# Kernel tuning notes

Measured on AMD Instinct MI355X. Metric: run time of the kernel, lower is better.

Reference implementation:

```python
import jax, jax.numpy as jnp
import numpy as np

D_MODEL, D_K, D_V, H = 1024, 64, 64, 16
B, NQ, NK = 4, 2048, 2048


def setup_inputs() -> dict:
    key = jax.random.key(0)
    ks = jax.random.split(key, 14)
    def xavier(k, fan_in, fan_out):
        lim = np.sqrt(6.0 / (fan_in + fan_out))
        return jax.random.uniform(k, (fan_in, fan_out), jnp.float32, -lim, lim)
    return {
        "queries": jax.random.normal(ks[0], (B, NQ, D_MODEL), jnp.float32),
        "keys": jax.random.normal(ks[1], (B, NK, D_MODEL), jnp.float32),
        "values": jax.random.normal(ks[2], (B, NK, D_MODEL), jnp.float32),
        "language_feature": jax.random.normal(ks[3], (B, NQ, D_MODEL), jnp.float32),
        "Wq": xavier(ks[4], D_MODEL, H * D_K), "bq": jnp.zeros((H * D_K,), jnp.float32),
        "Wk": xavier(ks[5], D_MODEL, H * D_K), "bk": jnp.zeros((H * D_K,), jnp.float32),
        "Wv": xavier(ks[6], D_MODEL, H * D_V), "bv": jnp.zeros((H * D_V,), jnp.float32),
        "Ws": xavier(ks[7], D_MODEL, H * D_K), "bs": jnp.zeros((H * D_K,), jnp.float32),
        "Wo": xavier(ks[8], H * D_V, D_MODEL), "bo": jnp.zeros((D_MODEL,), jnp.float32),
    }


def reference(queries, keys, values, language_feature, Wq, bq, Wk, bk, Wv, bv, Ws, bs, Wo, bo):
    b, nq = queries.shape[:2]
    nk = keys.shape[1]
    scale = 1.0 / np.sqrt(D_K)
    # projections -> [b, h, n, d]
    q = (queries @ Wq + bq).reshape(b, nq, H, D_K).transpose(0, 2, 1, 3)
    s = (language_feature @ Ws + bs).reshape(b, nq, H, D_K).transpose(0, 2, 1, 3)
    k = (keys @ Wk + bk).reshape(b, nk, H, D_K).transpose(0, 2, 1, 3)
    v = (values @ Wv + bv).reshape(b, nk, H, D_V).transpose(0, 2, 1, 3)
    # raw scaled scores [b, h, nq, nk]
    att = jnp.einsum("bhqd,bhkd->bhqk", q, k) * scale
    # language branch: per-query dot(q_i, s_i) -> [b, h, nq]
    lang = jnp.einsum("bhqd,bhqd->bhq", q, s) * scale
    # concatenated softmax over [nk + 1]; only last column (beta) is used
    combined = jax.nn.softmax(jnp.concatenate([att, lang[..., None]], axis=-1), axis=-1)
    beta = combined[..., -1:]  # [b, h, nq, 1]
    # NOTE: original uses RAW (non-softmaxed) att for the value aggregation
    att_v = jnp.einsum("bhqk,bhkd->bhqd", att, v)
    out = beta * s + (1.0 - beta) * att_v  # [b, h, nq, d]
    out = out.transpose(0, 2, 1, 3).reshape(b, nq, H * D_V)
    return out @ Wo + bo
```

## Files before the change

kernel.cpp:

```cpp
#include <hip/hip_runtime.h>


#define SCALE 0.125f
#define LOG2E 1.44269504088896f
#define SCLOG 0.18033688011112042f

typedef __attribute__((ext_vector_type(8))) short bf16x8;
typedef __attribute__((ext_vector_type(4))) short s16x4;
typedef __attribute__((ext_vector_type(4))) float f32x4;

__device__ __forceinline__ float b2f(short x) {
  return __uint_as_float(((unsigned)(unsigned short)x) << 16);
}
__device__ __forceinline__ short f2b(float x) {
  unsigned u = __float_as_uint(x);
  unsigned r = (u + 0x7fffu + ((u >> 16) & 1u)) >> 16;
  return (short)r;
}
__device__ __forceinline__ float fexp2(float x) {
  float r;
  asm("v_exp_f32 %0, %1" : "=v"(r) : "v"(x));
  return r;
}
__device__ __forceinline__ bf16x8 cvt8(f32x4 lo, f32x4 hi) {
  unsigned u0, u1, u2, u3;
  asm("v_cvt_pk_bf16_f32 %0, %1, %2" : "=v"(u0) : "v"(lo[0]), "v"(lo[1]));
  asm("v_cvt_pk_bf16_f32 %0, %1, %2" : "=v"(u1) : "v"(lo[2]), "v"(lo[3]));
  asm("v_cvt_pk_bf16_f32 %0, %1, %2" : "=v"(u2) : "v"(hi[0]), "v"(hi[1]));
  asm("v_cvt_pk_bf16_f32 %0, %1, %2" : "=v"(u3) : "v"(hi[2]), "v"(hi[3]));
  union { unsigned u[4]; bf16x8 v; } r;
  r.u[0] = u0; r.u[1] = u1; r.u[2] = u2; r.u[3] = u3;
  return r.v;
}

__device__ __forceinline__ void gl2lds16(const short* g, short* l) {
  __builtin_amdgcn_global_load_lds(
      (const __attribute__((address_space(1))) unsigned int*)g,
      (__attribute__((address_space(3))) unsigned int*)l, 16, 0, 0);
}

__global__ __launch_bounds__(256) void wtrans_kernel(
    const float* W0, const float* W1, const float* W2, const float* W3, const float* W4,
    short* O0, short* O1, short* O2, short* O3, short* O4) {
  const float* Wp[5] = {W0, W1, W2, W3, W4};
  short* Op[5] = {O0, O1, O2, O3, O4};
  const float* W = Wp[blockIdx.z];
  short* O = Op[blockIdx.z];
  int n0 = blockIdx.x * 64, k0 = blockIdx.y * 64;
  __shared__ float ts[64 * 68];
  int tid = threadIdx.x;
  int r = tid >> 4, c = (tid & 15) * 4;
  for (int ir = 0; ir < 4; ++ir) {
    f32x4 v = *reinterpret_cast<const f32x4*>(&W[(size_t)(k0 + r + ir * 16) * 1024 + n0 + c]);
    *reinterpret_cast<f32x4*>(&ts[(r + ir * 16) * 68 + c]) = v;
  }
  __syncthreads();
  for (int ir = 0; ir < 4; ++ir) {
    int n = r + ir * 16;
    s16x4 o;
    for (int j = 0; j < 4; ++j) o[j] = f2b(ts[(c + j) * 68 + n]);
    *reinterpret_cast<s16x4*>(&O[(size_t)(n0 + n) * 1024 + k0 + c]) = o;
  }
}


#define A_LOAD(T, R0, R1, R2, R3)                                           \
  {                                                                         \
    int kst = (T) * 32;                                                     \
    int row0 = tid >> 2, cc0 = tid & 3;                                     \
    int gc0 = (cc0 ^ ((row0 >> 1) & 3)) * 8;                                \
    const float* ap0 = &Ag[(size_t)(m0 + row0) * 1024 + kst + gc0];         \
    R0 = *reinterpret_cast<const f32x4*>(ap0);                              \
    R1 = *reinterpret_cast<const f32x4*>(ap0 + 4);                          \
    int row1 = row0 + 128;                                                  \
    int gc1 = (cc0 ^ ((row1 >> 1) & 3)) * 8;                                \
    const float* ap1 = &Ag[(size_t)(m0 + row1) * 1024 + kst + gc1];         \
    R2 = *reinterpret_cast<const f32x4*>(ap1);                              \
    R3 = *reinterpret_cast<const f32x4*>(ap1 + 4);                          \
  }

#define A_WRITE(T, R0, R1, R2, R3)                                          \
  {                                                                         \
    short* Ad = &As[(T) & 1][0];                                            \
    *reinterpret_cast<bf16x8*>(&Ad[tid * 8]) = cvt8(R0, R1);                \
    *reinterpret_cast<bf16x8*>(&Ad[(tid + 512) * 8]) = cvt8(R2, R3);        \
  }

#define B_STAGE(T)                                                          \
  {                                                                         \
    int kst = (T) * 32;                                                     \
    short* Bd = &Bs[(T) % 4][0];                                            \
    _Pragma("unroll") for (int it = 0; it < 2; ++it) {                      \
      int s = tid + it * 512;                                               \
      int row = s >> 2, cc = s & 3;                                         \
      int gc = (cc ^ ((row >> 1) & 3)) * 8;                                 \
      gl2lds16(&Bg[(size_t)(n0 + row) * 1024 + kst + gc], &Bd[s * 8]);      \
    }                                                                       \
  }

#define BODY(T, DO_STAGE, VM, DO_WRITE, W0, W1, W2, W3, L0, L1, L2, L3)     \
  {                                                                         \
    const short* Ab = &As[(T) & 1][0];                                      \
    const short* Bb = &Bs[(T) % 4][0];                                      \
    bf16x8 a[4], b[4];                                                      \
    _Pragma("unroll") for (int i = 0; i < 4; ++i) {                         \
      int r = wr + i * 16 + lr;                                             \
      a[i] = *reinterpret_cast<const bf16x8*>(                              \
          &Ab[r * 32 + ((lg ^ ((r >> 1) & 3)) * 8)]);                       \
    }                                                                       \
    _Pragma("unroll") for (int j = 0; j < 4; ++j) {                         \
      int rn = wc + j * 16 + lr;                                            \
      b[j] = *reinterpret_cast<const bf16x8*>(                              \
          &Bb[rn * 32 + ((lg ^ ((rn >> 1) & 3)) * 8)]);                     \
    }                                                                       \
    if (DO_STAGE) B_STAGE((T) + 3);                                         \
    __builtin_amdgcn_s_setprio(1);                                          \
    _Pragma("unroll") for (int j = 0; j < 4; ++j)                           \
      _Pragma("unroll") for (int i = 0; i < 4; ++i)                         \
        acc[i][j] = __builtin_amdgcn_mfma_f32_16x16x32_bf16(a[i], b[j], acc[i][j], 0, 0, 0); \
    __builtin_amdgcn_s_setprio(0);                                          \
    __builtin_amdgcn_s_barrier();                                           \
    bf16x8 a2[4];                                                           \
    _Pragma("unroll") for (int i = 0; i < 4; ++i) {                         \
      int r = wr + 64 + i * 16 + lr;                                        \
      a2[i] = *reinterpret_cast<const bf16x8*>(                             \
          &Ab[r * 32 + ((lg ^ ((r >> 1) & 3)) * 8)]);                       \
    }                                                                       \
    if (DO_STAGE) A_LOAD((T) + 3, L0, L1, L2, L3);                          \
    asm volatile("s_waitcnt vmcnt(" #VM ")" ::: "memory");                  \
    if (DO_WRITE) A_WRITE((T) + 1, W0, W1, W2, W3);                         \
    __builtin_amdgcn_s_setprio(1);                                          \
    _Pragma("unroll") for (int j = 0; j < 4; ++j)                           \
      _Pragma("unroll") for (int i = 0; i < 4; ++i)                         \
        acc[i + 4][j] = __builtin_amdgcn_mfma_f32_16x16x32_bf16(a2[i], b[j], acc[i + 4][j], 0, 0, 0); \
    __builtin_amdgcn_s_setprio(0);                                          \
    asm volatile("s_waitcnt lgkmcnt(0)" ::: "memory");                      \
    __builtin_amdgcn_s_barrier();                                           \
  }

#define GEMM_CORE()                                                         \
  f32x4 p0, p1, p2, p3, q0, q1, q2, q3, r0, r1, r2, r3;                     \
  B_STAGE(0); A_LOAD(0, p0, p1, p2, p3);                                    \
  B_STAGE(1); A_LOAD(1, q0, q1, q2, q3);                                    \
  B_STAGE(2); A_LOAD(2, r0, r1, r2, r3);                                    \
  asm volatile("s_waitcnt vmcnt(12)" ::: "memory");                         \
  A_WRITE(0, p0, p1, p2, p3);                                               \
  asm volatile("s_waitcnt lgkmcnt(0)" ::: "memory");                        \
  __builtin_amdgcn_s_barrier();                                             \
  for (int t = 0; t < 27; t += 3) {                                         \
    BODY(t, true, 12, true, q0, q1, q2, q3, p0, p1, p2, p3);                \
    BODY(t + 1, true, 12, true, r0, r1, r2, r3, q0, q1, q2, q3);            \
    BODY(t + 2, true, 12, true, p0, p1, p2, p3, r0, r1, r2, r3);            \
  }                                                                         \
  BODY(27, true, 12, true, q0, q1, q2, q3, p0, p1, p2, p3);                 \
  BODY(28, true, 12, true, r0, r1, r2, r3, q0, q1, q2, q3);                 \
  BODY(29, false, 6, true, p0, p1, p2, p3, p0, p1, p2, p3);                 \
  BODY(30, false, 0, true, q0, q1, q2, q3, p0, p1, p2, p3);                 \
  BODY(31, false, 0, false, p0, p1, p2, p3, p0, p1, p2, p3);

__global__ __launch_bounds__(512, 2) void proj_gemm_kernel(
    const float* A0, const float* A1, const float* A2, const float* A3,
    const short* W0, const short* W1, const short* W2, const short* W3,
    const float* c0, const float* c1, const float* c2, const float* c3,
    short* O0, short* O1, short* O2, short* O3) {
  const float* Ap[4] = {A0, A1, A2, A3};
  const short* Wp[4] = {W0, W1, W2, W3};
  const float* bp[4] = {c0, c1, c2, c3};
  short* Op[4] = {O0, O1, O2, O3};

  int id = blockIdx.x;
  int work = (id & 7) * 64 + (id >> 3);
  int z = work >> 7;
  int rem = work & 127;
  int my = rem >> 2;
  int nx = rem & 3;
  const float* Ag = Ap[z];
  const short* Bg = Wp[z];
  const float* bias = bp[z];
  short* Out = Op[z];
  int m0 = my * 256, n0 = nx * 256;

  __shared__ short As[2][8192];
  __shared__ short Bs[4][8192];
  int tid = threadIdx.x;
  int wave = tid >> 6, lane = tid & 63, lg = lane >> 4, lr = lane & 15;
  int wr = (wave >> 2) * 128, wc = (wave & 3) * 64;

  f32x4 acc[8][4] = {};

  GEMM_CORE();

#pragma unroll
  for (int j = 0; j < 4; ++j) {
    int n = n0 + wc + j * 16 + lr;
    float bi = bias[n];
    int hh = n >> 6, d = n & 63;
#pragma unroll
    for (int i = 0; i < 8; ++i)
      for (int rr = 0; rr < 4; ++rr) {
        int m = m0 + wr + i * 16 + lg * 4 + rr;
        int bb = m >> 11, t = m & 2047;
        Out[(size_t)(((bb << 4) + hh) * 2048 + t) * 64 + d] = f2b(acc[i][j][rr] + bi);
      }
  }
}

__global__ __launch_bounds__(256) void final_gemm_kernel(const short* A, const short* Wt,
                                                         const float* bias, float* Out) {
  int id = blockIdx.x;
  int work = (id & 7) * 64 + (id >> 3);
  int my = work >> 3, nx = work & 7;
  int m0 = my * 128, n0 = nx * 128;

  __shared__ short Asl[128 * 64];
  __shared__ short Bsl[128 * 64];
  int tid = threadIdx.x;
  int wave = tid >> 6, lane = tid & 63, lg = lane >> 4, lr = lane & 15;
  int wr = (wave >> 1) * 64, wc = (wave & 1) * 64;
  f32x4 acc[4][4] = {};
  int srow = lane >> 3, scol = (lane & 7) * 8;

  for (int k0 = 0; k0 < 1024; k0 += 64) {
    __syncthreads();
#pragma unroll
    for (int i = 0; i < 4; ++i) {
      int c = i * 4 + wave;
      gl2lds16(&A[(size_t)(m0 + c * 8 + srow) * 1024 + k0 + scol], &Asl[c * 512 + lane * 8]);
      gl2lds16(&Wt[(size_t)(n0 + c * 8 + srow) * 1024 + k0 + scol], &Bsl[c * 512 + lane * 8]);
    }
    __syncthreads();
#pragma unroll
    for (int kk = 0; kk < 2; ++kk) {
      bf16x8 a[4], b[4];
      for (int i = 0; i < 4; ++i)
        a[i] = *reinterpret_cast<const bf16x8*>(&Asl[(wr + i * 16 + lr) * 64 + kk * 32 + lg * 8]);
      for (int j = 0; j < 4; ++j)
        b[j] = *reinterpret_cast<const bf16x8*>(&Bsl[(wc + j * 16 + lr) * 64 + kk * 32 + lg * 8]);
      for (int i = 0; i < 4; ++i)
        for (int j = 0; j < 4; ++j)
          acc[i][j] = __builtin_amdgcn_mfma_f32_16x16x32_bf16(a[i], b[j], acc[i][j], 0, 0, 0);
    }
  }
  for (int j = 0; j < 4; ++j) {
    int n = n0 + wc + j * 16 + lr;
    float bi = bias[n];
    for (int i = 0; i < 4; ++i)
      for (int rr = 0; rr < 4; ++rr) {
        int m = m0 + wr + i * 16 + lg * 4 + rr;
        Out[(size_t)m * 1024 + n] = acc[i][j][rr] + bi;
      }
  }
}

__global__ __launch_bounds__(256) void kv_kernel(const short* Kp, const short* Vp, float* KVp) {
  int c = blockIdx.x, bh = blockIdx.y;
  int tid = threadIdx.x;
  __shared__ float Ks[32 * 64];
  __shared__ float Vs[32 * 64];
  int srow = tid >> 3, scol = (tid & 7) * 8;
  int dk = tid >> 2, dv0 = (tid & 3) * 16;
  float acc[16] = {};
  for (int sub = 0; sub < 8; ++sub) {
    int tkb = c * 256 + sub * 32;
    __syncthreads();
    bf16x8 kv = *reinterpret_cast<const bf16x8*>(&Kp[(size_t)(bh * 2048 + tkb + srow) * 64 + scol]);
    bf16x8 vv = *reinterpret_cast<const bf16x8*>(&Vp[(size_t)(bh * 2048 + tkb + srow) * 64 + scol]);
    f32x4 ka, kb, va, vb;
#pragma unroll
    for (int j = 0; j < 4; ++j) {
      ka[j] = b2f(kv[j]); kb[j] = b2f(kv[j + 4]);
      va[j] = b2f(vv[j]); vb[j] = b2f(vv[j + 4]);
    }
    *reinterpret_cast<f32x4*>(&Ks[srow * 64 + scol]) = ka;
    *reinterpret_cast<f32x4*>(&Ks[srow * 64 + scol + 4]) = kb;
    *reinterpret_cast<f32x4*>(&Vs[srow * 64 + scol]) = va;
    *reinterpret_cast<f32x4*>(&Vs[srow * 64 + scol + 4]) = vb;
    __syncthreads();
    for (int tok = 0; tok < 32; ++tok) {
      float kval = Ks[tok * 64 + dk];
      f32x4 v0 = *reinterpret_cast<const f32x4*>(&Vs[tok * 64 + dv0]);
      f32x4 v1 = *reinterpret_cast<const f32x4*>(&Vs[tok * 64 + dv0 + 4]);
      f32x4 v2 = *reinterpret_cast<const f32x4*>(&Vs[tok * 64 + dv0 + 8]);
      f32x4 v3 = *reinterpret_cast<const f32x4*>(&Vs[tok * 64 + dv0 + 12]);
#pragma unroll
      for (int j = 0; j < 4; ++j) {
        acc[j] += kval * v0[j];
        acc[4 + j] += kval * v1[j];
        acc[8 + j] += kval * v2[j];
        acc[12 + j] += kval * v3[j];
      }
    }
  }
  float* o = &KVp[(size_t)(bh * 8 + c) * 4096 + dk * 64 + dv0];
  for (int j = 0; j < 16; ++j) o[j] = acc[j];
}

__global__ __launch_bounds__(256) void kvred_kernel(const float* KVp, short* KVt) {
  int bh = blockIdx.x;
  for (int e = threadIdx.x; e < 4096; e += 256) {
    float s = 0.f;
    for (int cc = 0; cc < 8; ++cc) s += KVp[(size_t)(bh * 8 + cc) * 4096 + e];
    int dk = e >> 6, dv = e & 63;
    KVt[(size_t)bh * 4096 + dv * 64 + dk] = f2b(s);
  }
}

__global__ __launch_bounds__(256) void beta_combine_kernel(
    const short* Qp, const short* Kp, const short* Sp, const short* KVt, short* X) {
  int bh = blockIdx.y, q0 = blockIdx.x * 64;
  int b = bh >> 4, h = bh & 15;
  int tid = threadIdx.x;
  __shared__ float lsm[64];
  __shared__ short Ks[2][128 * 64];

  const short* Kb = Kp + (size_t)bh * 2048 * 64;
  int srow = tid >> 3, schunk = tid & 7;
  int sxor = (schunk ^ (srow & 7)) * 8;

#pragma unroll
  for (int cc = 0; cc < 4; ++cc)
    gl2lds16(&Kb[(size_t)(cc * 32 + srow) * 64 + sxor], &Ks[0][cc * 2048 + tid * 8]);

  {
    int row = tid >> 2, seg = tid & 3;
    const short* qr = Qp + (size_t)(bh * 2048 + q0 + row) * 64 + seg * 16;
    const short* sr = Sp + (size_t)(bh * 2048 + q0 + row) * 64 + seg * 16;
    float sum = 0.f;
    for (int cc = 0; cc < 2; ++cc) {
      bf16x8 qv = reinterpret_cast<const bf16x8*>(qr)[cc];
      bf16x8 sv = reinterpret_cast<const bf16x8*>(sr)[cc];
      for (int j = 0; j < 8; ++j) sum += b2f(qv[j]) * b2f(sv[j]);
    }
    sum += __shfl_xor(sum, 1);
    sum += __shfl_xor(sum, 2);
    if (seg == 0) lsm[row] = sum * SCLOG;
  }
  __syncthreads();

  int wave = tid >> 6, lane = tid & 63, lg = lane >> 4, lr = lane & 15;
  int qrow = q0 + wave * 16 + lr;
  const bf16x8* qbase = reinterpret_cast<const bf16x8*>(Qp + (size_t)(bh * 2048 + qrow) * 64);
  bf16x8 a0 = qbase[lg];
  bf16x8 a1 = qbase[4 + lg];
  bf16x8 as0, as1;
#pragma unroll
  for (int j = 0; j < 8; ++j) {
    as0[j] = f2b(b2f(a0[j]) * SCLOG);
    as1[j] = f2b(b2f(a1[j]) * SCLOG);
  }

  float s0 = 0.f, s1 = 0.f, s2 = 0.f, s3 = 0.f;
  for (int t = 0; t < 16; ++t) {
    __builtin_amdgcn_s_barrier();
    if (t < 15) {
      const short* src = Kb + (size_t)(t + 1) * 8192;
      short* dst = &Ks[(t + 1) & 1][0];
#pragma unroll
      for (int cc = 0; cc < 4; ++cc)
        gl2lds16(&src[(size_t)(cc * 32 + srow) * 64 + sxor], &dst[cc * 2048 + tid * 8]);
      asm volatile("s_waitcnt vmcnt(4)" ::: "memory");
    } else {
      asm volatile("s_waitcnt vmcnt(0)" ::: "memory");
    }
    __builtin_amdgcn_s_barrier();
    __builtin_amdgcn_sched_barrier(0);
    const short* Kbuf = &Ks[t & 1][0];
    f32x4 sc[8];
    __builtin_amdgcn_s_setprio(1);
#pragma unroll
    for (int nt = 0; nt < 8; ++nt) {
      int row = nt * 16 + lr;
      int xs = row & 7;
      bf16x8 b0 = *reinterpret_cast<const bf16x8*>(&Kbuf[row * 64 + ((lg ^ xs) * 8)]);
      bf16x8 b1 = *reinterpret_cast<const bf16x8*>(&Kbuf[row * 64 + (((4 + lg) ^ xs) * 8)]);
      f32x4 z = {0.f, 0.f, 0.f, 0.f};
      z = __builtin_amdgcn_mfma_f32_16x16x32_bf16(as0, b0, z, 0, 0, 0);
      z = __builtin_amdgcn_mfma_f32_16x16x32_bf16(as1, b1, z, 0, 0, 0);
      sc[nt] = z;
    }
    __builtin_amdgcn_s_setprio(0);
#pragma unroll
    for (int nt = 0; nt < 8; ++nt) {
      s0 += fexp2(sc[nt][0]);
      s1 += fexp2(sc[nt][1]);
      s2 += fexp2(sc[nt][2]);
      s3 += fexp2(sc[nt][3]);
    }
  }
  for (int m = 1; m < 16; m <<= 1) {
    s0 += __shfl_xor(s0, m);
    s1 += __shfl_xor(s1, m);
    s2 += __shfl_xor(s2, m);
    s3 += __shfl_xor(s3, m);
  }
  float bt[4];
  {
    float sarr[4] = {s0, s1, s2, s3};
#pragma unroll
    for (int rr = 0; rr < 4; ++rr) {
      int rl = wave * 16 + lg * 4 + rr;
      float el = fexp2(lsm[rl]);
      bt[rr] = el / (sarr[rr] + el);
    }
  }
  const short* kvb = KVt + (size_t)bh * 4096;
#pragma unroll
  for (int nt = 0; nt < 4; ++nt) {
    const bf16x8* bb8 = reinterpret_cast<const bf16x8*>(&kvb[(nt * 16 + lr) * 64]);
    bf16x8 b0 = bb8[lg], b1 = bb8[4 + lg];
    f32x4 z = {0.f, 0.f, 0.f, 0.f};
    z = __builtin_amdgcn_mfma_f32_16x16x32_bf16(a0, b0, z, 0, 0, 0);
    z = __builtin_amdgcn_mfma_f32_16x16x32_bf16(a1, b1, z, 0, 0, 0);
#pragma unroll
    for (int rr = 0; rr < 4; ++rr) {
      int rl = wave * 16 + lg * 4 + rr;
      int q = q0 + rl;
      float sv = b2f(Sp[(size_t)(bh * 2048 + q) * 64 + nt * 16 + lr]);
      float val = bt[rr] * sv + (1.0f - bt[rr]) * (SCALE * z[rr]);
      X[(size_t)(b * 2048 + q) * 1024 + h * 64 + nt * 16 + lr] = f2b(val);
    }
  }
}

extern "C" void kernel_launch(void* const* d_in, const int* in_sizes, int n_in,
                              void* d_out, int out_size, void* d_ws, size_t ws_size,
                              hipStream_t stream) {
  const float* queries = (const float*)d_in[0];
  const float* keys = (const float*)d_in[1];
  const float* values = (const float*)d_in[2];
  const float* langf = (const float*)d_in[3];
  const float* Wq = (const float*)d_in[4];
  const float* bq = (const float*)d_in[5];
  const float* Wk = (const float*)d_in[6];
  const float* bk = (const float*)d_in[7];
  const float* Wv = (const float*)d_in[8];
  const float* bv = (const float*)d_in[9];
  const float* Ws = (const float*)d_in[10];
  const float* bs = (const float*)d_in[11];
  const float* Wo = (const float*)d_in[12];
  const float* bo = (const float*)d_in[13];
  float* out = (float*)d_out;

  char* ws = (char*)d_ws;
  const size_t MB = 1ull << 20;
  short* Wqt = (short*)(ws + 0 * MB);
  short* Wkt = (short*)(ws + 2 * MB);
  short* Wvt = (short*)(ws + 4 * MB);
  short* Wst = (short*)(ws + 6 * MB);
  short* Wot = (short*)(ws + 8 * MB);
  short* Qp = (short*)(ws + 10 * MB);
  short* Kp = (short*)(ws + 26 * MB);
  short* Vp = (short*)(ws + 42 * MB);
  short* Sp = (short*)(ws + 58 * MB);
  short* X = (short*)(ws + 74 * MB);
  float* KVp = (float*)(ws + 90 * MB);
  short* KVt = (short*)(ws + 98 * MB);

  wtrans_kernel<<<dim3(16, 16, 5), 256, 0, stream>>>(Wq, Wk, Wv, Ws, Wo, Wqt, Wkt, Wvt, Wst, Wot);
  proj_gemm_kernel<<<512, 512, 0, stream>>>(queries, keys, values, langf,
                                            Wqt, Wkt, Wvt, Wst, bq, bk, bv, bs,
                                            Qp, Kp, Vp, Sp);
  kv_kernel<<<dim3(8, 64), 256, 0, stream>>>(Kp, Vp, KVp);
  kvred_kernel<<<64, 256, 0, stream>>>(KVp, KVt);
  beta_combine_kernel<<<dim3(32, 64), 256, 0, stream>>>(Qp, Kp, Sp, KVt, X);
  final_gemm_kernel<<<512, 256, 0, stream>>>(X, Wot, bo, out);
}
```

Measured before the change: 229.4 us.

## Split beta score tiles by key slice per wave and reduce across waves

```diff
diff --git a/kernel.cpp b/kernel.cpp
--- a/kernel.cpp
+++ b/kernel.cpp
@@ -62,7 +62,6 @@
     *reinterpret_cast<s16x4*>(&O[(size_t)(n0 + n) * 1024 + k0 + c]) = o;
   }
 }
-
 
 #define A_LOAD(T, R0, R1, R2, R3)                                           \
   {                                                                         \
@@ -311,6 +310,8 @@
   int b = bh >> 4, h = bh & 15;
   int tid = threadIdx.x;
   __shared__ float lsm[64];
+  __shared__ float red[4][64];
+  __shared__ float betaL[64];
   __shared__ short Ks[2][128 * 64];
 
   const short* Kb = Kp + (size_t)bh * 2048 * 64;
@@ -338,18 +339,24 @@
   __syncthreads();
 
   int wave = tid >> 6, lane = tid & 63, lg = lane >> 4, lr = lane & 15;
-  int qrow = q0 + wave * 16 + lr;
-  const bf16x8* qbase = reinterpret_cast<const bf16x8*>(Qp + (size_t)(bh * 2048 + qrow) * 64);
+  const bf16x8* qbase = reinterpret_cast<const bf16x8*>(
+      Qp + (size_t)(bh * 2048 + q0 + wave * 16 + lr) * 64);
   bf16x8 a0 = qbase[lg];
   bf16x8 a1 = qbase[4 + lg];
-  bf16x8 as0, as1;
-#pragma unroll
-  for (int j = 0; j < 8; ++j) {
-    as0[j] = f2b(b2f(a0[j]) * SCLOG);
-    as1[j] = f2b(b2f(a1[j]) * SCLOG);
-  }
-
-  float s0 = 0.f, s1 = 0.f, s2 = 0.f, s3 = 0.f;
+  bf16x8 as0[4], as1[4];
+#pragma unroll
+  for (int qt = 0; qt < 4; ++qt) {
+    const bf16x8* qb = reinterpret_cast<const bf16x8*>(
+        Qp + (size_t)(bh * 2048 + q0 + qt * 16 + lr) * 64);
+    bf16x8 t0 = qb[lg], t1 = qb[4 + lg];
+#pragma unroll
+    for (int j = 0; j < 8; ++j) {
+      as0[qt][j] = f2b(b2f(t0[j]) * SCLOG);
+      as1[qt][j] = f2b(b2f(t1[j]) * SCLOG);
+    }
+  }
+
+  float s[4][4] = {};
   for (int t = 0; t < 16; ++t) {
     __builtin_amdgcn_s_barrier();
     if (t < 15) {
@@ -365,44 +372,56 @@
     __builtin_amdgcn_s_barrier();
     __builtin_amdgcn_sched_barrier(0);
     const short* Kbuf = &Ks[t & 1][0];
-    f32x4 sc[8];
+    f32x4 sc[4][2];
     __builtin_amdgcn_s_setprio(1);
 #pragma unroll
-    for (int nt = 0; nt < 8; ++nt) {
-      int row = nt * 16 + lr;
+    for (int kt = 0; kt < 2; ++kt) {
+      int row = wave * 32 + kt * 16 + lr;
       int xs = row & 7;
       bf16x8 b0 = *reinterpret_cast<const bf16x8*>(&Kbuf[row * 64 + ((lg ^ xs) * 8)]);
       bf16x8 b1 = *reinterpret_cast<const bf16x8*>(&Kbuf[row * 64 + (((4 + lg) ^ xs) * 8)]);
-      f32x4 z = {0.f, 0.f, 0.f, 0.f};
-      z = __builtin_amdgcn_mfma_f32_16x16x32_bf16(as0, b0, z, 0, 0, 0);
-      z = __builtin_amdgcn_mfma_f32_16x16x32_bf16(as1, b1, z, 0, 0, 0);
-      sc[nt] = z;
+#pragma unroll
+      for (int qt = 0; qt < 4; ++qt) {
+        f32x4 z = {0.f, 0.f, 0.f, 0.f};
+        z = __builtin_amdgcn_mfma_f32_16x16x32_bf16(as0[qt], b0, z, 0, 0, 0);
+        z = __builtin_amdgcn_mfma_f32_16x16x32_bf16(as1[qt], b1, z, 0, 0, 0);
+        sc[qt][kt] = z;
+      }
     }
     __builtin_amdgcn_s_setprio(0);
 #pragma unroll
-    for (int nt = 0; nt < 8; ++nt) {
-      s0 += fexp2(sc[nt][0]);
-      s1 += fexp2(sc[nt][1]);
-      s2 += fexp2(sc[nt][2]);
-      s3 += fexp2(sc[nt][3]);
-    }
-  }
-  for (int m = 1; m < 16; m <<= 1) {
-    s0 += __shfl_xor(s0, m);
-    s1 += __shfl_xor(s1, m);
-    s2 += __shfl_xor(s2, m);
-    s3 += __shfl_xor(s3, m);
-  }
+    for (int qt = 0; qt < 4; ++qt)
+#pragma unroll
+      for (int kt = 0; kt < 2; ++kt) {
+        s[qt][0] += fexp2(sc[qt][kt][0]);
+        s[qt][1] += fexp2(sc[qt][kt][1]);
+        s[qt][2] += fexp2(sc[qt][kt][2]);
+        s[qt][3] += fexp2(sc[qt][kt][3]);
+      }
+  }
+#pragma unroll
+  for (int qt = 0; qt < 4; ++qt)
+#pragma unroll
+    for (int rr = 0; rr < 4; ++rr)
+      for (int m = 1; m < 16; m <<= 1) s[qt][rr] += __shfl_xor(s[qt][rr], m);
+  if (lr == 0) {
+#pragma unroll
+    for (int qt = 0; qt < 4; ++qt)
+#pragma unroll
+      for (int rr = 0; rr < 4; ++rr)
+        red[wave][qt * 16 + lg * 4 + rr] = s[qt][rr];
+  }
+  __syncthreads();
+  if (tid < 64) {
+    float tot = red[0][tid] + red[1][tid] + red[2][tid] + red[3][tid];
+    float el = fexp2(lsm[tid]);
+    betaL[tid] = el / (tot + el);
+  }
+  __syncthreads();
   float bt[4];
-  {
-    float sarr[4] = {s0, s1, s2, s3};
-#pragma unroll
-    for (int rr = 0; rr < 4; ++rr) {
-      int rl = wave * 16 + lg * 4 + rr;
-      float el = fexp2(lsm[rl]);
-      bt[rr] = el / (sarr[rr] + el);
-    }
-  }
+#pragma unroll
+  for (int rr = 0; rr < 4; ++rr) bt[rr] = betaL[wave * 16 + lg * 4 + rr];
+
   const short* kvb = KVt + (size_t)bh * 4096;
 #pragma unroll
   for (int nt = 0; nt < 4; ++nt) {
```

Result: no change. 229.2 us (-0.1%).
